# Optimization experiments

Measured on AMD Instinct MI355X. Metric: run time of the kernel, lower is better.

The kernel has to match this reference:

```python
import math
import jax, jax.numpy as jnp
import numpy as np

B, S, D = 8, 920, 1536
H, HD = 4, 384            # num heads, head dim; all_head = H*HD = 1536
MAX_POS = 920
L = 2 * MAX_POS - 1       # 1839 relative positions


def setup_inputs() -> dict:
    key = jax.random.key(0)
    k1, k2, k3, k4, k5 = jax.random.split(key, 5)
    return {
        "hidden_states": jax.random.normal(k1, (B, S, D), dtype=jnp.float32),
        "w_query": jax.random.normal(k2, (D, H * HD), dtype=jnp.float32) * 0.02,
        "w_key": jax.random.normal(k3, (D, H * HD), dtype=jnp.float32) * 0.02,
        "w_value": jax.random.normal(k4, (D, H * HD), dtype=jnp.float32) * 0.02,
        "distance_embedding": jax.random.normal(k5, (L, HD), dtype=jnp.float32) * 0.02,
    }


def reshape_fortran(x, shape):
    # Matches torch reference: reverse-permute, C reshape of reversed shape, reverse-permute back.
    x = jnp.transpose(x, tuple(reversed(range(x.ndim))))
    x = jnp.reshape(x, tuple(reversed(shape)))
    return jnp.transpose(x, tuple(reversed(range(len(shape)))))


def relative_position_embedding_rotate(scores):
    # scores: [B, H, L, S]
    scores = jnp.transpose(scores, (0, 2, 3, 1))  # [B, L, S, H]
    b, hs, s, h = scores.shape
    scores = jnp.concatenate([scores, jnp.zeros((b, s, s, h), scores.dtype)], axis=1)
    scores = reshape_fortran(scores, [b, (hs + s) * s, 1, h])
    scores = scores[:, : (s + hs - 1) * s]
    scores = reshape_fortran(scores, [b, hs + s - 1, s, h])
    halfpoint = hs // 2
    scores = scores[:, halfpoint : halfpoint + s]          # [B, S, S, H]
    scores = jnp.transpose(scores, (0, 2, 1, 3))           # transpose(1,2)
    return jnp.transpose(scores, (0, 3, 1, 2))             # [B, H, S, S]


def reference(hidden_states, w_query, w_key, w_value, distance_embedding):
    inv = 1.0 / math.sqrt(HD)
    q = (hidden_states @ w_query) * inv                    # [B, S, H*HD]
    k = hidden_states @ w_key
    v = hidden_states @ w_value

    def heads(x):  # [B,S,H*HD] -> [B,H,S,HD]
        return jnp.transpose(x.reshape(B, S, H, HD), (0, 2, 1, 3))

    q, k, v = heads(q), heads(k), heads(v)

    scores = jnp.einsum("bhqd,bhkd->bhqk", q, k)           # [B,H,S,S]
    rel = jnp.einsum("ld,bhsd->bhls", distance_embedding, q)  # [B,H,L,S]
    scores = scores + relative_position_embedding_rotate(rel)

    probs = jax.nn.softmax(scores, axis=-1)
    ctx = jnp.einsum("bhqk,bhkd->bhqd", probs, v)          # [B,H,S,HD]
    ctx = jnp.transpose(ctx, (0, 2, 1, 3)).reshape(B, S, H * HD)
    return ctx
```

## Files before the change

### kernel.cpp

```cpp
#include <hip/hip_runtime.h>

#define S_LEN 920
#define DMODEL 1536
#define NH 4
#define HD 384
#define LREL 1839
#define BATCH 8
#define MTOT (BATCH * S_LEN)
#define KPAD 960
#define NBH (BATCH * NH)

#define CHS   5652480UL
#define BSLAB 2826240UL
#define KOFF  1413120UL

#define EB_BYTES 1412352UL
#define VT_BYTES 23592960UL

typedef __attribute__((ext_vector_type(8))) short  s16x8;
typedef __attribute__((ext_vector_type(4))) short  s16x4;
typedef __attribute__((ext_vector_type(8))) __bf16 bf16x8;
typedef __attribute__((ext_vector_type(4))) float  f32x4;

__device__ __forceinline__ short f2b(float x) {
  unsigned u = __builtin_bit_cast(unsigned, x);
  unsigned r = (u + 0x7FFFu + ((u >> 16) & 1u)) >> 16;
  return (short)r;
}
__device__ __forceinline__ float b2f(short s) {
  unsigned u = ((unsigned)(unsigned short)s) << 16;
  return __builtin_bit_cast(float, u);
}

__device__ __forceinline__ void load_lds16(const short* g, short* lds) {
  __builtin_amdgcn_global_load_lds(
      (const __attribute__((address_space(1))) void*)g,
      (__attribute__((address_space(3))) void*)lds, 16, 0, 0);
}

__device__ __forceinline__ f32x4 mfma_bf16(s16x8 a, s16x8 b, f32x4 c) {
  return __builtin_amdgcn_mfma_f32_16x16x32_bf16(
      __builtin_bit_cast(bf16x8, a), __builtin_bit_cast(bf16x8, b), c, 0, 0, 0);
}

__device__ __forceinline__ s16x8 frag_swz(const short* base, int row, int kk, int lq) {
  int byte = (row << 7) + (kk << 6) + (lq << 4);
  byte ^= (row & 7) << 4;
  return *(const s16x8*)((const char*)base + byte);
}

template <int NT>
__device__ __forceinline__ void gemm_pipe(short* smem,
    const short* __restrict__ A, int ldA, int mClamp, int m0,
    const short* __restrict__ B, int ldB, int nClamp, int n0,
    f32x4 acc[4][6]) {
  short* const A0 = smem;
  short* const B0 = smem + 16384;
  short* const A1 = smem + 28672;
  short* const B1 = smem + 45056;

  const int tid = threadIdx.x, w = tid >> 6, lane = tid & 63;
  const int lr = lane & 15, lq = lane >> 4;
  const int wr = w >> 1, wc = w & 1;

  const short* pa[4]; int la[4];
  const short* pb[3]; int lb[3];
  {
    const int rl = lane >> 3, c = lane & 7;
#pragma unroll
    for (int i = 0; i < 4; ++i) {
      int r = w * 32 + i * 8 + rl;
      int ra = m0 + r; if (ra > mClamp) ra = mClamp;
      pa[i] = A + (size_t)ra * ldA + ((c ^ (r & 7)) * 8);
      la[i] = (w * 32 + i * 8) * 64;
    }
#pragma unroll
    for (int i = 0; i < 3; ++i) {
      int r = w * 24 + i * 8 + rl;
      int rb = n0 + r; if (rb > nClamp) rb = nClamp;
      pb[i] = B + (size_t)rb * ldB + ((c ^ (r & 7)) * 8);
      lb[i] = (w * 24 + i * 8) * 64;
    }
  }

#pragma unroll
  for (int i = 0; i < 4; ++i)
#pragma unroll
    for (int j = 0; j < 6; ++j) acc[i][j] = (f32x4){0.f, 0.f, 0.f, 0.f};

#pragma unroll
  for (int i = 0; i < 4; ++i) load_lds16(pa[i], A0 + la[i]);
#pragma unroll
  for (int i = 0; i < 3; ++i) load_lds16(pb[i], B0 + lb[i]);

  for (int kt = 0; kt < NT; ++kt) {
    short* const Ab = (kt & 1) ? A1 : A0;
    short* const Bb = (kt & 1) ? B1 : B0;
    short* const An = (kt & 1) ? A0 : A1;
    short* const Bn = (kt & 1) ? B0 : B1;

    if (kt + 1 < NT) {
      const int k0 = (kt + 1) * 64;
#pragma unroll
      for (int i = 0; i < 4; ++i) load_lds16(pa[i] + k0, An + la[i]);
#pragma unroll
      for (int i = 0; i < 3; ++i) load_lds16(pb[i] + k0, Bn + lb[i]);
      asm volatile("s_waitcnt vmcnt(7)" ::: "memory");
    } else {
      asm volatile("s_waitcnt vmcnt(0)" ::: "memory");
    }
    __builtin_amdgcn_sched_barrier(0);
    __builtin_amdgcn_s_barrier();
    __builtin_amdgcn_sched_barrier(0);

    s16x8 a[4], bb[3];
#pragma unroll
    for (int f = 0; f < 4; ++f) a[f] = frag_swz(Ab, wr * 64 + f * 16 + lr, 0, lq);
#pragma unroll
    for (int f = 0; f < 3; ++f) bb[f] = frag_swz(Bb, wc * 96 + f * 16 + lr, 0, lq);
    __builtin_amdgcn_s_barrier();
    __builtin_amdgcn_s_setprio(1);
#pragma unroll
    for (int i = 0; i < 4; ++i)
#pragma unroll
      for (int j = 0; j < 3; ++j) acc[i][j] = mfma_bf16(a[i], bb[j], acc[i][j]);
    __builtin_amdgcn_s_setprio(0);
    __builtin_amdgcn_s_barrier();
#pragma unroll
    for (int f = 0; f < 3; ++f) bb[f] = frag_swz(Bb, wc * 96 + (3 + f) * 16 + lr, 0, lq);
    __builtin_amdgcn_s_barrier();
    __builtin_amdgcn_s_setprio(1);
#pragma unroll
    for (int i = 0; i < 4; ++i)
#pragma unroll
      for (int j = 0; j < 3; ++j) acc[i][3 + j] = mfma_bf16(a[i], bb[j], acc[i][3 + j]);
    __builtin_amdgcn_s_setprio(0);
    __builtin_amdgcn_s_barrier();
#pragma unroll
    for (int f = 0; f < 4; ++f) a[f] = frag_swz(Ab, wr * 64 + f * 16 + lr, 1, lq);
#pragma unroll
    for (int f = 0; f < 3; ++f) bb[f] = frag_swz(Bb, wc * 96 + f * 16 + lr, 1, lq);
    __builtin_amdgcn_s_barrier();
    __builtin_amdgcn_s_setprio(1);
#pragma unroll
    for (int i = 0; i < 4; ++i)
#pragma unroll
      for (int j = 0; j < 3; ++j) acc[i][j] = mfma_bf16(a[i], bb[j], acc[i][j]);
    __builtin_amdgcn_s_setprio(0);
    __builtin_amdgcn_s_barrier();
#pragma unroll
    for (int f = 0; f < 3; ++f) bb[f] = frag_swz(Bb, wc * 96 + (3 + f) * 16 + lr, 1, lq);
    __builtin_amdgcn_s_barrier();
    __builtin_amdgcn_s_setprio(1);
#pragma unroll
    for (int i = 0; i < 4; ++i)
#pragma unroll
      for (int j = 0; j < 3; ++j) acc[i][3 + j] = mfma_bf16(a[i], bb[j], acc[i][3 + j]);
    __builtin_amdgcn_s_setprio(0);
    __builtin_amdgcn_s_barrier();
  }
}

__global__ void k_cast(const float* __restrict__ X, short* __restrict__ O, int n4) {
  int i = blockIdx.x * blockDim.x + threadIdx.x;
  if (i >= n4) return;
  float4 v = ((const float4*)X)[i];
  s16x4 o = {f2b(v.x), f2b(v.y), f2b(v.z), f2b(v.w)};
  *(s16x4*)&O[(size_t)i * 4] = o;
}

__global__ void k_transpose_w(const float* __restrict__ W0, const float* __restrict__ W1,
                              const float* __restrict__ W2, short* __restrict__ Wt) {
  const float* W = (blockIdx.z == 0) ? W0 : ((blockIdx.z == 1) ? W1 : W2);
  short* O = Wt + (size_t)blockIdx.z * DMODEL * DMODEL;
  __shared__ float t[32][33];
  int tx = threadIdx.x, ty = threadIdx.y;
  int n0 = blockIdx.x * 32, k0 = blockIdx.y * 32;
#pragma unroll
  for (int i = 0; i < 4; ++i)
    t[ty + i * 8][tx] = W[(size_t)(k0 + ty + i * 8) * DMODEL + n0 + tx];
  __syncthreads();
#pragma unroll
  for (int i = 0; i < 4; ++i)
    O[(size_t)(n0 + ty + i * 8) * DMODEL + k0 + tx] = f2b(t[tx][ty + i * 8]);
}

__global__ void k_zero_vtpad(short* __restrict__ Vt) {
  int idx = blockIdx.x * blockDim.x + threadIdx.x;
  if (idx >= NBH * HD * (KPAD - S_LEN)) return;
  int bhd = idx / (KPAD - S_LEN);
  int s = S_LEN + idx - bhd * (KPAD - S_LEN);
  Vt[(size_t)bhd * KPAD + s] = 0;
}

#define QKV_NT (DMODEL / 64)

__global__ __launch_bounds__(512, 2) void k_gemm_qkv(const short* __restrict__ Xb,
                                                     const short* __restrict__ Wt,
                                                     short* __restrict__ out16,
                                                     short* __restrict__ Vt) {
  __shared__ short smem[57344];
  const int z = blockIdx.z;
  const int t = blockIdx.x;
  const int t2 = (t & 7) * 29 + (t >> 3);
  const int m0 = (t2 >> 3) * 256;
  const int n0 = (t2 & 7) * 192;

  const int tid = threadIdx.x, w = tid >> 6, lane = tid & 63;
  const int lr = lane & 15, lq = lane >> 4;
  const int wr = w >> 1, wc = w & 1;

  f32x4 acc[4][6];
  gemm_pipe<QKV_NT>(smem, Xb, DMODEL, MTOT - 1, m0,
                    Wt + (size_t)z * DMODEL * DMODEL, DMODEL, DMODEL - 1, n0, acc);

  __syncthreads();
  const float inv = 0.05103103630798287f;
  if (z != 2) {
    short* T = smem;
#pragma unroll
    for (int i = 0; i < 4; ++i)
#pragma unroll
      for (int j = 0; j < 6; ++j) {
        int ml = wr * 64 + i * 16 + lq * 4;
        int nl = wc * 96 + j * 16 + lr;
#pragma unroll
        for (int r = 0; r < 4; ++r) {
          float v = acc[i][j][r];
          T[(ml + r) * 200 + nl] = f2b(z == 0 ? v * inv : v);
        }
      }
    __syncthreads();
    for (int u = 0; u < 12; ++u) {
      int unit = u * 512 + tid;
      int ml = unit / 24, c = unit - ml * 24;
      int m = m0 + ml;
      if (m < MTOT) {
        int b = m / S_LEN, s = m - b * S_LEN;
        short* dst = out16 + (size_t)(b >> 1) * CHS + (size_t)(b & 1) * BSLAB +
                     (z == 1 ? KOFF : 0UL) + (size_t)s * DMODEL + n0 + c * 8;
        *(s16x8*)dst = *(const s16x8*)&T[ml * 200 + c * 8];
      }
    }
  } else {
    short* T = smem;
#pragma unroll
    for (int i = 0; i < 4; ++i)
#pragma unroll
      for (int j = 0; j < 6; ++j) {
        int ml = wr * 64 + i * 16 + lq * 4;
        int nl = wc * 96 + j * 16 + lr;
#pragma unroll
        for (int r = 0; r < 4; ++r)
          T[nl * 264 + ml + r] = f2b(acc[i][j][r]);
      }
    __syncthreads();
    const int h = n0 / HD;
    const int d0 = n0 - h * HD;
    for (int u = 0; u < 12; ++u) {
      int unit = u * 512 + tid;
      int nl = unit >> 5, c = unit & 31;
      int m = m0 + c * 8;
      if (m < MTOT) {
        int b = m / S_LEN, s = m - b * S_LEN;
        size_t row = (size_t)(b * NH + h) * HD + d0 + nl;
        *(s16x8*)&Vt[row * KPAD + s] = *(const s16x8*)&T[nl * 264 + c * 8];
      }
    }
  }
}

#define FKV 192
#define FNT 5

#define WAITVM(N) { asm volatile("s_waitcnt vmcnt(" #N ")" ::: "memory"); \
  __builtin_amdgcn_sched_barrier(0); __builtin_amdgcn_s_barrier(); \
  __builtin_amdgcn_sched_barrier(0); }

#define LBAR { asm volatile("s_waitcnt lgkmcnt(0)" ::: "memory"); \
  __builtin_amdgcn_sched_barrier(0); __builtin_amdgcn_s_barrier(); \
  __builtin_amdgcn_sched_barrier(0); }

#define NOISSUE { }

#define STAGE_E(BUF, C, L0) { \
  _Pragma("unroll") for (int i_ = 0; i_ < 4; ++i_) { \
    int r_ = w * 32 + i_ * 8 + rl; \
    int rg_ = (L0) + r_; rg_ = rg_ < 0 ? 0 : (rg_ > LREL - 1 ? LREL - 1 : rg_); \
    load_lds16(Eb + (size_t)rg_ * HD + ((cs ^ (r_ & 7)) * 8) + (C) * 64, \
               (BUF) + (w * 32 + i_ * 8) * 64); } }

#define STAGE_K(BUF, C) { \
  _Pragma("unroll") for (int i_ = 0; i_ < 3; ++i_) { \
    int r_ = w * 24 + i_ * 8 + rl; \
    int rg_ = kv0 + r_; if (rg_ > S_LEN - 1) rg_ = S_LEN - 1; \
    load_lds16(Kp + (size_t)rg_ * DMODEL + ((cs ^ (r_ & 7)) * 8) + (C) * 64, \
               (BUF) + (w * 24 + i_ * 8) * 64); } }

#define STAGE_V(BUF, HF, SC) { \
  _Pragma("unroll") for (int i_ = 0; i_ < 3; ++i_) { \
    int r_ = w * 24 + i_ * 8 + rl; \
    load_lds16(Vb + (size_t)((HF) * 192 + r_) * KPAD + kv0 + (SC) * 64 + ((cs ^ (r_ & 7)) * 8), \
               (BUF) + (w * 24 + i_ * 8) * 64); } }

#define GSLOT_T(CUR, C, ISSUE, WVM) { ISSUE; WVM; \
  s16x8 a_[2][2], b_[2][4]; \
  _Pragma("unroll") for (int k_ = 0; k_ < 2; ++k_) { \
    _Pragma("unroll") for (int i_ = 0; i_ < 2; ++i_) \
      a_[i_][k_] = frag_swz(QL + (C) * 4096, wm * 32 + i_ * 16 + lr, k_, lq); \
    _Pragma("unroll") for (int j_ = 0; j_ < 4; ++j_) \
      b_[k_][j_] = frag_swz((CUR), wn * 64 + j_ * 16 + lr, k_, lq); } \
  __builtin_amdgcn_s_setprio(1); \
  _Pragma("unroll") for (int k_ = 0; k_ < 2; ++k_) \
    _Pragma("unroll") for (int i_ = 0; i_ < 2; ++i_) \
      _Pragma("unroll") for (int j_ = 0; j_ < 4; ++j_) \
        acc_t[i_][j_] = mfma_bf16(a_[i_][k_], b_[k_][j_], acc_t[i_][j_]); \
  __builtin_amdgcn_s_setprio(0); __builtin_amdgcn_s_barrier(); }

#define GSLOT_S(CUR, C, ISSUE, WVM) { ISSUE; WVM; \
  s16x8 a_[2][2], b_[2][3]; \
  _Pragma("unroll") for (int k_ = 0; k_ < 2; ++k_) { \
    _Pragma("unroll") for (int i_ = 0; i_ < 2; ++i_) \
      a_[i_][k_] = frag_swz(QL + (C) * 4096, wm * 32 + i_ * 16 + lr, k_, lq); \
    _Pragma("unroll") for (int j_ = 0; j_ < 3; ++j_) \
      b_[k_][j_] = frag_swz((CUR), wn * 48 + j_ * 16 + lr, k_, lq); } \
  __builtin_amdgcn_s_setprio(1); \
  _Pragma("unroll") for (int k_ = 0; k_ < 2; ++k_) \
    _Pragma("unroll") for (int i_ = 0; i_ < 2; ++i_) \
      _Pragma("unroll") for (int j_ = 0; j_ < 3; ++j_) \
        acc_s[i_][j_] = mfma_bf16(a_[i_][k_], b_[k_][j_], acc_s[i_][j_]); \
  __builtin_amdgcn_s_setprio(0); __builtin_amdgcn_s_barrier(); }

#define GSLOT_PV(CUR, SC, HF, ISSUE, WVM) { ISSUE; WVM; \
  s16x8 a_[2][2], b_[2][3]; \
  _Pragma("unroll") for (int k_ = 0; k_ < 2; ++k_) { \
    _Pragma("unroll") for (int i_ = 0; i_ < 2; ++i_) \
      a_[i_][k_] = frag_swz(TLP + (SC) * 4096, wm * 32 + i_ * 16 + lr, k_, lq); \
    _Pragma("unroll") for (int j_ = 0; j_ < 3; ++j_) \
      b_[k_][j_] = frag_swz((CUR), wn * 48 + j_ * 16 + lr, k_, lq); } \
  __builtin_amdgcn_s_setprio(1); \
  _Pragma("unroll") for (int k_ = 0; k_ < 2; ++k_) \
    _Pragma("unroll") for (int i_ = 0; i_ < 2; ++i_) \
      _Pragma("unroll") for (int j_ = 0; j_ < 3; ++j_) \
        acc_o[i_][(HF) * 3 + j_] = mfma_bf16(a_[i_][k_], b_[k_][j_], acc_o[i_][(HF) * 3 + j_]); \
  __builtin_amdgcn_s_setprio(0); __builtin_amdgcn_s_barrier(); }

__global__ __launch_bounds__(512, 1) void k_fused(const short* __restrict__ out16,
                                                  const short* __restrict__ Vt,
                                                  const short* __restrict__ Eb,
                                                  float* __restrict__ O, int half) {
  __shared__ short smem[74752];
  short* const QL  = smem;
  short* const B0  = smem + 24576;
  short* const B1  = smem + 40960;
  short* const TLP = smem + 57344;
  float* const pmax = (float*)(smem + 73728);
  float* const psum = pmax + 256;

  const int f  = blockIdx.x;
  const int f2 = (f & 7) * 30 + (f >> 3);
  const int mt = f2 % 15, bhl = f2 / 15;
  const int bh = half * 16 + bhl, b = bh >> 2, h = bh & 3;
  const int m0 = mt * 64;

  const int tid = threadIdx.x, w = tid >> 6, lane = tid & 63;
  const int lr = lane & 15, lq = lane >> 4;
  const int wm = w >> 2, wn = w & 3;
  const int rl = lane >> 3, cs = lane & 7;

  const short* Qp = out16 + (size_t)(b >> 1) * CHS + (size_t)(b & 1) * BSLAB + h * HD;
  const short* Kp = Qp + KOFF;
  const short* Vb = Vt + (size_t)bh * HD * KPAD;
  float* Ob = O + (size_t)bhl * S_LEN * HD;

  f32x4 acc_o[2][6];
  float Mst[2][4], Lst[2][4];
#pragma unroll
  for (int i = 0; i < 2; ++i) {
#pragma unroll
    for (int j = 0; j < 6; ++j) acc_o[i][j] = (f32x4){0.f, 0.f, 0.f, 0.f};
#pragma unroll
    for (int r = 0; r < 4; ++r) { Mst[i][r] = -1e30f; Lst[i][r] = 0.f; }
  }

#pragma unroll
  for (int i = 0; i < 6; ++i) {
    int rq = w * 8 + rl;
    int rg = m0 + rq; if (rg > S_LEN - 1) rg = S_LEN - 1;
    load_lds16(Qp + (size_t)rg * DMODEL + ((cs ^ (rq & 7)) * 8) + i * 64,
               QL + i * 4096 + (w * 8) * 64);
  }
  { const int l0p = 856 - m0; STAGE_E(B0, 0, l0p); }

  for (int t = 0; t < FNT; ++t) {
    const int kv0 = t * FKV;
    const int l0 = kv0 - m0 + 856;

    f32x4 acc_t[2][4];
#pragma unroll
    for (int i = 0; i < 2; ++i)
#pragma unroll
      for (int j = 0; j < 4; ++j) acc_t[i][j] = (f32x4){0.f, 0.f, 0.f, 0.f};

    GSLOT_T(B0, 0, STAGE_E(B1, 1, l0), WAITVM(4));
    GSLOT_T(B1, 1, STAGE_E(B0, 2, l0), WAITVM(4));
    GSLOT_T(B0, 2, STAGE_E(B1, 3, l0), WAITVM(4));
    GSLOT_T(B1, 3, STAGE_E(B0, 4, l0), WAITVM(4));
    GSLOT_T(B0, 4, STAGE_E(B1, 5, l0), WAITVM(4));
    GSLOT_T(B1, 5, STAGE_K(B0, 0),     WAITVM(3));

#pragma unroll
    for (int i = 0; i < 2; ++i)
#pragma unroll
      for (int j = 0; j < 4; ++j)
#pragma unroll
        for (int r = 0; r < 4; ++r) {
          int row = wm * 32 + i * 16 + lq * 4 + r;
          int col = wn * 64 + j * 16 + lr;
          TLP[row * 256 + col] = f2b(acc_t[i][j][r]);
        }
    LBAR;

    f32x4 acc_s[2][3];
#pragma unroll
    for (int i = 0; i < 2; ++i)
#pragma unroll
      for (int j = 0; j < 3; ++j) acc_s[i][j] = (f32x4){0.f, 0.f, 0.f, 0.f};

    GSLOT_S(B0, 0, STAGE_K(B1, 1), WAITVM(3));
    GSLOT_S(B1, 1, STAGE_K(B0, 2), WAITVM(3));
    GSLOT_S(B0, 2, STAGE_K(B1, 3), WAITVM(3));
    GSLOT_S(B1, 3, STAGE_K(B0, 4), WAITVM(3));
    GSLOT_S(B0, 4, STAGE_K(B1, 5), WAITVM(3));
    GSLOT_S(B1, 5, STAGE_V(B0, 0, 0), WAITVM(3));

#pragma unroll
    for (int i = 0; i < 2; ++i)
#pragma unroll
      for (int j = 0; j < 3; ++j) {
        int jpl = wn * 48 + j * 16 + lr;
        int jp = kv0 + jpl;
#pragma unroll
        for (int r = 0; r < 4; ++r) {
          int row = wm * 32 + i * 16 + lq * 4 + r;
          float x = acc_s[i][j][r] + b2f(TLP[row * 256 + (jpl - row + 63)]);
          acc_s[i][j][r] = (jp < S_LEN) ? x : -1e30f;
        }
      }
    {
      float tm[2][4];
#pragma unroll
      for (int i = 0; i < 2; ++i)
#pragma unroll
        for (int r = 0; r < 4; ++r) {
          float v = fmaxf(fmaxf(acc_s[i][0][r], acc_s[i][1][r]), acc_s[i][2][r]);
#pragma unroll
          for (int o = 1; o < 16; o <<= 1) v = fmaxf(v, __shfl_xor(v, o));
          tm[i][r] = v;
        }
      if (lr == 0) {
#pragma unroll
        for (int i = 0; i < 2; ++i)
#pragma unroll
          for (int r = 0; r < 4; ++r)
            pmax[wn * 64 + wm * 32 + i * 16 + lq * 4 + r] = tm[i][r];
      }
    }
    LBAR;
    float fexp[2][4], ps[2][4];
#pragma unroll
    for (int i = 0; i < 2; ++i)
#pragma unroll
      for (int r = 0; r < 4; ++r) {
        int row = wm * 32 + i * 16 + lq * 4 + r;
        float M2 = fmaxf(fmaxf(pmax[row], pmax[64 + row]),
                         fmaxf(pmax[128 + row], pmax[192 + row]));
        M2 = fmaxf(M2, Mst[i][r]);
        fexp[i][r] = __expf(Mst[i][r] - M2);
        Mst[i][r] = M2;
      }
#pragma unroll
    for (int i = 0; i < 2; ++i)
#pragma unroll
      for (int r = 0; r < 4; ++r) {
        float s0 = 0.f;
#pragma unroll
        for (int j = 0; j < 3; ++j) {
          float p = __expf(acc_s[i][j][r] - Mst[i][r]);
          acc_s[i][j][r] = p;
          s0 += p;
        }
#pragma unroll
        for (int o = 1; o < 16; o <<= 1) s0 += __shfl_xor(s0, o);
        ps[i][r] = s0;
#pragma unroll
        for (int jj = 0; jj < 6; ++jj) acc_o[i][jj][r] *= fexp[i][r];
      }
    if (lr == 0) {
#pragma unroll
      for (int i = 0; i < 2; ++i)
#pragma unroll
        for (int r = 0; r < 4; ++r)
          psum[wn * 64 + wm * 32 + i * 16 + lq * 4 + r] = ps[i][r];
    }
    LBAR;
#pragma unroll
    for (int i = 0; i < 2; ++i)
#pragma unroll
      for (int r = 0; r < 4; ++r) {
        int row = wm * 32 + i * 16 + lq * 4 + r;
        float ts = psum[row] + psum[64 + row] + psum[128 + row] + psum[192 + row];
        Lst[i][r] = Lst[i][r] * fexp[i][r] + ts;
      }
#pragma unroll
    for (int i = 0; i < 2; ++i)
#pragma unroll
      for (int j = 0; j < 3; ++j) {
        int c192 = wn * 48 + j * 16 + lr;
        int sc = c192 >> 6, c64 = c192 & 63;
#pragma unroll
        for (int r = 0; r < 4; ++r) {
          int row = wm * 32 + i * 16 + lq * 4 + r;
          int byte = sc * 8192 + row * 128 + ((c64 * 2) ^ ((row & 7) * 16));
          *(short*)((char*)TLP + byte) = f2b(acc_s[i][j][r]);
        }
      }
    LBAR;

    GSLOT_PV(B0, 0, 0, STAGE_V(B1, 0, 1), WAITVM(3));
    GSLOT_PV(B1, 1, 0, STAGE_V(B0, 0, 2), WAITVM(3));
    GSLOT_PV(B0, 2, 0, STAGE_V(B1, 1, 0), WAITVM(3));
    GSLOT_PV(B1, 0, 1, STAGE_V(B0, 1, 1), WAITVM(3));
    GSLOT_PV(B0, 1, 1, STAGE_V(B1, 1, 2), WAITVM(3));
    if (t < FNT - 1) {
      GSLOT_PV(B1, 2, 1, STAGE_E(B0, 0, l0 + FKV), WAITVM(4));
    } else {
      GSLOT_PV(B1, 2, 1, NOISSUE, WAITVM(0));
    }
  }

#pragma unroll
  for (int i = 0; i < 2; ++i)
#pragma unroll
    for (int r = 0; r < 4; ++r) {
      int m = m0 + wm * 32 + i * 16 + lq * 4 + r;
      if (m < S_LEN) {
        float rs = 1.0f / Lst[i][r];
#pragma unroll
        for (int jj = 0; jj < 6; ++jj) {
          int d = (jj / 3) * 192 + wn * 48 + (jj % 3) * 16 + lr;
          Ob[(size_t)m * HD + d] = acc_o[i][jj][r] * rs;
        }
      }
    }
}

__global__ __launch_bounds__(256) void k_copy_o(const float* __restrict__ O,
                                                float* __restrict__ out, int b0) {
  int i = blockIdx.x * 256 + threadIdx.x;
  if (i >= 16 * S_LEN * HD / 4) return;
  const int per_bh = S_LEN * HD / 4;
  int bhl = i / per_bh, rem = i - bhl * per_bh;
  int m = rem / (HD / 4), d4 = rem - m * (HD / 4);
  int b = b0 + (bhl >> 2), h = bhl & 3;
  float4 v = ((const float4*)O)[i];
  ((float4*)out)[((size_t)(b * S_LEN + m) * DMODEL + h * HD + d4 * 4) >> 2] = v;
}

extern "C" void kernel_launch(void* const* d_in, const int* in_sizes, int n_in,
                              void* d_out, int out_size, void* d_ws, size_t ws_size,
                              hipStream_t stream) {
  const float* hs = (const float*)d_in[0];
  const float* wq = (const float*)d_in[1];
  const float* wk = (const float*)d_in[2];
  const float* wv = (const float*)d_in[3];
  const float* de = (const float*)d_in[4];
  char* ws = (char*)d_ws;

  short* Xb = (short*)(ws + 0);
  short* Wt = (short*)(ws + 22609920UL);
  short* Eb = (short*)(ws + 36765696UL);
  short* Vt = (short*)(ws + 36765696UL + EB_BYTES);
  float* Og = (float*)(ws + 0);
  short* out16 = (short*)d_out;

  k_cast<<<(MTOT * DMODEL / 4 + 255) / 256, 256, 0, stream>>>(hs, Xb, MTOT * DMODEL / 4);
  k_cast<<<(LREL * HD / 4 + 255) / 256, 256, 0, stream>>>(de, Eb, LREL * HD / 4);
  k_transpose_w<<<dim3(48, 48, 3), dim3(32, 8, 1), 0, stream>>>(wq, wk, wv, Wt);
  k_zero_vtpad<<<(NBH * HD * (KPAD - S_LEN) + 255) / 256, 256, 0, stream>>>(Vt);

  k_gemm_qkv<<<dim3(232, 1, 3), 512, 0, stream>>>(Xb, Wt, out16, Vt);

  for (int hf = 0; hf < 2; ++hf) {
    k_fused<<<dim3(240), 512, 0, stream>>>(out16, Vt, Eb, Og, hf);
    k_copy_o<<<dim3(5520), 256, 0, stream>>>(Og, (float*)d_out, hf * 4);
  }
}
```

Measured before the change: 423.1 us.

## Hold Q fragments in registers and triple-buffer LDS staging for deeper prefetch

Q is now loaded once straight from global memory into registers as MFMA fragments, instead of being staged in LDS and re-read with frag_swz in every slot. The LDS this frees pays for a third staging buffer, so E/K/V chunks are prefetched two slots ahead and the vmcnt waits are loosened to match. The goal is to hide global load latency better and to cut LDS read traffic for Q. The cost is heavy register pressure from 24 s16x8 Q fragments held for the whole kernel, which risks spills.

```diff
diff --git a/kernel.cpp b/kernel.cpp
--- a/kernel.cpp
+++ b/kernel.cpp
@@ -283,61 +283,57 @@
 
 #define NOISSUE { }
 
-#define STAGE_E(BUF, C, L0) { \
+#define STAGE_E(BUF_, C, L0) { \
   _Pragma("unroll") for (int i_ = 0; i_ < 4; ++i_) { \
     int r_ = w * 32 + i_ * 8 + rl; \
     int rg_ = (L0) + r_; rg_ = rg_ < 0 ? 0 : (rg_ > LREL - 1 ? LREL - 1 : rg_); \
     load_lds16(Eb + (size_t)rg_ * HD + ((cs ^ (r_ & 7)) * 8) + (C) * 64, \
-               (BUF) + (w * 32 + i_ * 8) * 64); } }
-
-#define STAGE_K(BUF, C) { \
+               (BUF_) + (w * 32 + i_ * 8) * 64); } }
+
+#define STAGE_K(BUF_, C) { \
   _Pragma("unroll") for (int i_ = 0; i_ < 3; ++i_) { \
     int r_ = w * 24 + i_ * 8 + rl; \
     int rg_ = kv0 + r_; if (rg_ > S_LEN - 1) rg_ = S_LEN - 1; \
     load_lds16(Kp + (size_t)rg_ * DMODEL + ((cs ^ (r_ & 7)) * 8) + (C) * 64, \
-               (BUF) + (w * 24 + i_ * 8) * 64); } }
-
-#define STAGE_V(BUF, HF, SC) { \
+               (BUF_) + (w * 24 + i_ * 8) * 64); } }
+
+#define STAGE_V(BUF_, HF, SC) { \
   _Pragma("unroll") for (int i_ = 0; i_ < 3; ++i_) { \
     int r_ = w * 24 + i_ * 8 + rl; \
     load_lds16(Vb + (size_t)((HF) * 192 + r_) * KPAD + kv0 + (SC) * 64 + ((cs ^ (r_ & 7)) * 8), \
-               (BUF) + (w * 24 + i_ * 8) * 64); } }
-
-#define GSLOT_T(CUR, C, ISSUE, WVM) { ISSUE; WVM; \
-  s16x8 a_[2][2], b_[2][4]; \
-  _Pragma("unroll") for (int k_ = 0; k_ < 2; ++k_) { \
-    _Pragma("unroll") for (int i_ = 0; i_ < 2; ++i_) \
-      a_[i_][k_] = frag_swz(QL + (C) * 4096, wm * 32 + i_ * 16 + lr, k_, lq); \
+               (BUF_) + (w * 24 + i_ * 8) * 64); } }
+
+#define SLOT_T(C, BUFR, ISSUE, WVM) { ISSUE; WVM; \
+  s16x8 b_[2][4]; \
+  _Pragma("unroll") for (int k_ = 0; k_ < 2; ++k_) \
     _Pragma("unroll") for (int j_ = 0; j_ < 4; ++j_) \
-      b_[k_][j_] = frag_swz((CUR), wn * 64 + j_ * 16 + lr, k_, lq); } \
+      b_[k_][j_] = frag_swz((BUFR), wn * 64 + j_ * 16 + lr, k_, lq); \
   __builtin_amdgcn_s_setprio(1); \
   _Pragma("unroll") for (int k_ = 0; k_ < 2; ++k_) \
     _Pragma("unroll") for (int i_ = 0; i_ < 2; ++i_) \
       _Pragma("unroll") for (int j_ = 0; j_ < 4; ++j_) \
-        acc_t[i_][j_] = mfma_bf16(a_[i_][k_], b_[k_][j_], acc_t[i_][j_]); \
+        acc_t[i_][j_] = mfma_bf16(q[C][i_][k_], b_[k_][j_], acc_t[i_][j_]); \
   __builtin_amdgcn_s_setprio(0); __builtin_amdgcn_s_barrier(); }
 
-#define GSLOT_S(CUR, C, ISSUE, WVM) { ISSUE; WVM; \
-  s16x8 a_[2][2], b_[2][3]; \
-  _Pragma("unroll") for (int k_ = 0; k_ < 2; ++k_) { \
-    _Pragma("unroll") for (int i_ = 0; i_ < 2; ++i_) \
-      a_[i_][k_] = frag_swz(QL + (C) * 4096, wm * 32 + i_ * 16 + lr, k_, lq); \
+#define SLOT_S(C, BUFR, ISSUE, WVM) { ISSUE; WVM; \
+  s16x8 b_[2][3]; \
+  _Pragma("unroll") for (int k_ = 0; k_ < 2; ++k_) \
     _Pragma("unroll") for (int j_ = 0; j_ < 3; ++j_) \
-      b_[k_][j_] = frag_swz((CUR), wn * 48 + j_ * 16 + lr, k_, lq); } \
+      b_[k_][j_] = frag_swz((BUFR), wn * 48 + j_ * 16 + lr, k_, lq); \
   __builtin_amdgcn_s_setprio(1); \
   _Pragma("unroll") for (int k_ = 0; k_ < 2; ++k_) \
     _Pragma("unroll") for (int i_ = 0; i_ < 2; ++i_) \
       _Pragma("unroll") for (int j_ = 0; j_ < 3; ++j_) \
-        acc_s[i_][j_] = mfma_bf16(a_[i_][k_], b_[k_][j_], acc_s[i_][j_]); \
+        acc_s[i_][j_] = mfma_bf16(q[C][i_][k_], b_[k_][j_], acc_s[i_][j_]); \
   __builtin_amdgcn_s_setprio(0); __builtin_amdgcn_s_barrier(); }
 
-#define GSLOT_PV(CUR, SC, HF, ISSUE, WVM) { ISSUE; WVM; \
+#define SLOT_PV(SC, HF, BUFR, ISSUE, WVM) { ISSUE; WVM; \
   s16x8 a_[2][2], b_[2][3]; \
   _Pragma("unroll") for (int k_ = 0; k_ < 2; ++k_) { \
     _Pragma("unroll") for (int i_ = 0; i_ < 2; ++i_) \
       a_[i_][k_] = frag_swz(TLP + (SC) * 4096, wm * 32 + i_ * 16 + lr, k_, lq); \
     _Pragma("unroll") for (int j_ = 0; j_ < 3; ++j_) \
-      b_[k_][j_] = frag_swz((CUR), wn * 48 + j_ * 16 + lr, k_, lq); } \
+      b_[k_][j_] = frag_swz((BUFR), wn * 48 + j_ * 16 + lr, k_, lq); } \
   __builtin_amdgcn_s_setprio(1); \
   _Pragma("unroll") for (int k_ = 0; k_ < 2; ++k_) \
     _Pragma("unroll") for (int i_ = 0; i_ < 2; ++i_) \
@@ -349,12 +345,12 @@
                                                   const short* __restrict__ Vt,
                                                   const short* __restrict__ Eb,
                                                   float* __restrict__ O, int half) {
-  __shared__ short smem[74752];
-  short* const QL  = smem;
-  short* const B0  = smem + 24576;
-  short* const B1  = smem + 40960;
-  short* const TLP = smem + 57344;
-  float* const pmax = (float*)(smem + 73728);
+  __shared__ short smem[66560];
+  short* const B0h = smem;
+  short* const B1h = smem + 16384;
+  short* const B2h = smem + 32768;
+  short* const TLP = smem + 49152;
+  float* const pmax = (float*)(smem + 65536);
   float* const psum = pmax + 256;
 
   const int f  = blockIdx.x;
@@ -383,14 +379,17 @@
     for (int r = 0; r < 4; ++r) { Mst[i][r] = -1e30f; Lst[i][r] = 0.f; }
   }
 
-#pragma unroll
-  for (int i = 0; i < 6; ++i) {
-    int rq = w * 8 + rl;
-    int rg = m0 + rq; if (rg > S_LEN - 1) rg = S_LEN - 1;
-    load_lds16(Qp + (size_t)rg * DMODEL + ((cs ^ (rq & 7)) * 8) + i * 64,
-               QL + i * 4096 + (w * 8) * 64);
-  }
-  { const int l0p = 856 - m0; STAGE_E(B0, 0, l0p); }
+  s16x8 q[6][2][2];
+#pragma unroll
+  for (int c = 0; c < 6; ++c)
+#pragma unroll
+    for (int i = 0; i < 2; ++i) {
+      int rg = m0 + wm * 32 + i * 16 + lr; if (rg > S_LEN - 1) rg = S_LEN - 1;
+#pragma unroll
+      for (int k = 0; k < 2; ++k)
+        q[c][i][k] = *(const s16x8*)(Qp + (size_t)rg * DMODEL + c * 64 + k * 32 + lq * 8);
+    }
+  { const int l00 = 856 - m0; STAGE_E(B0h, 0, l00); STAGE_E(B1h, 1, l00); }
 
   for (int t = 0; t < FNT; ++t) {
     const int kv0 = t * FKV;
@@ -402,12 +401,12 @@
 #pragma unroll
       for (int j = 0; j < 4; ++j) acc_t[i][j] = (f32x4){0.f, 0.f, 0.f, 0.f};
 
-    GSLOT_T(B0, 0, STAGE_E(B1, 1, l0), WAITVM(4));
-    GSLOT_T(B1, 1, STAGE_E(B0, 2, l0), WAITVM(4));
-    GSLOT_T(B0, 2, STAGE_E(B1, 3, l0), WAITVM(4));
-    GSLOT_T(B1, 3, STAGE_E(B0, 4, l0), WAITVM(4));
-    GSLOT_T(B0, 4, STAGE_E(B1, 5, l0), WAITVM(4));
-    GSLOT_T(B1, 5, STAGE_K(B0, 0),     WAITVM(3));
+    SLOT_T(0, B0h, STAGE_E(B2h, 2, l0), WAITVM(8));
+    SLOT_T(1, B1h, STAGE_E(B0h, 3, l0), WAITVM(8));
+    SLOT_T(2, B2h, STAGE_E(B1h, 4, l0), WAITVM(8));
+    SLOT_T(3, B0h, STAGE_E(B2h, 5, l0), WAITVM(8));
+    SLOT_T(4, B1h, STAGE_K(B0h, 0),     WAITVM(7));
+    SLOT_T(5, B2h, STAGE_K(B1h, 1),     WAITVM(6));
 
 #pragma unroll
     for (int i = 0; i < 2; ++i)
@@ -427,12 +426,12 @@
 #pragma unroll
       for (int j = 0; j < 3; ++j) acc_s[i][j] = (f32x4){0.f, 0.f, 0.f, 0.f};
 
-    GSLOT_S(B0, 0, STAGE_K(B1, 1), WAITVM(3));
-    GSLOT_S(B1, 1, STAGE_K(B0, 2), WAITVM(3));
-    GSLOT_S(B0, 2, STAGE_K(B1, 3), WAITVM(3));
-    GSLOT_S(B1, 3, STAGE_K(B0, 4), WAITVM(3));
-    GSLOT_S(B0, 4, STAGE_K(B1, 5), WAITVM(3));
-    GSLOT_S(B1, 5, STAGE_V(B0, 0, 0), WAITVM(3));
+    SLOT_S(0, B0h, STAGE_K(B2h, 2),       WAITVM(6));
+    SLOT_S(1, B1h, STAGE_K(B0h, 3),       WAITVM(6));
+    SLOT_S(2, B2h, STAGE_K(B1h, 4),       WAITVM(6));
+    SLOT_S(3, B0h, STAGE_K(B2h, 5),       WAITVM(6));
+    SLOT_S(4, B1h, STAGE_V(B0h, 0, 0),    WAITVM(6));
+    SLOT_S(5, B2h, STAGE_V(B1h, 0, 1),    WAITVM(6));
 
 #pragma unroll
     for (int i = 0; i < 2; ++i)
@@ -527,15 +526,16 @@
       }
     LBAR;
 
-    GSLOT_PV(B0, 0, 0, STAGE_V(B1, 0, 1), WAITVM(3));
-    GSLOT_PV(B1, 1, 0, STAGE_V(B0, 0, 2), WAITVM(3));
-    GSLOT_PV(B0, 2, 0, STAGE_V(B1, 1, 0), WAITVM(3));
-    GSLOT_PV(B1, 0, 1, STAGE_V(B0, 1, 1), WAITVM(3));
-    GSLOT_PV(B0, 1, 1, STAGE_V(B1, 1, 2), WAITVM(3));
+    SLOT_PV(0, 0, B0h, STAGE_V(B2h, 0, 2), WAITVM(6));
+    SLOT_PV(1, 0, B1h, STAGE_V(B0h, 1, 0), WAITVM(6));
+    SLOT_PV(2, 0, B2h, STAGE_V(B1h, 1, 1), WAITVM(6));
+    SLOT_PV(0, 1, B0h, STAGE_V(B2h, 1, 2), WAITVM(6));
     if (t < FNT - 1) {
-      GSLOT_PV(B1, 2, 1, STAGE_E(B0, 0, l0 + FKV), WAITVM(4));
+      SLOT_PV(1, 1, B1h, STAGE_E(B0h, 0, l0 + FKV), WAITVM(7));
+      SLOT_PV(2, 1, B2h, STAGE_E(B1h, 1, l0 + FKV), WAITVM(8));
     } else {
-      GSLOT_PV(B1, 2, 1, NOISSUE, WAITVM(0));
+      SLOT_PV(1, 1, B1h, NOISSUE, WAITVM(3));
+      SLOT_PV(2, 1, B2h, NOISSUE, WAITVM(0));
     }
   }
 
```

Result: slower. 623.9 us (+47.5%).
